# Optimization experiments

Measured on AMD Instinct MI355X. Metric: run time of the kernel, lower is better.

Reference implementation:

```python
import jax, jax.numpy as jnp
import numpy as np

B, C, H, W, NA = 2, 512, 25, 25, 9
A = H * W * NA  # 5625 anchors
PROB_T = 0.5
OVL_T = 0.5


def _make_anchors():
    ys, xs = np.meshgrid(np.arange(H), np.arange(W), indexing='ij')
    cx = (xs + 0.5) / W
    cy = (ys + 0.5) / H
    boxes = []
    for s in (0.1, 0.2, 0.4):
        for r in (0.5, 1.0, 2.0):
            w = s * np.sqrt(r)
            h = s / np.sqrt(r)
            boxes.append(np.stack([cx - w / 2, cy - h / 2, cx + w / 2, cy + h / 2], -1))
    anc = np.stack(boxes, axis=2)  # [H, W, 9, 4] matches [B,H,W,9*4] reshape order
    return jnp.asarray(anc.reshape(-1, 4), jnp.float32)


def setup_inputs() -> dict:
    key = jax.random.key(0)
    ks = jax.random.split(key, 4)
    x = jax.random.normal(ks[0], (B, C, H, W), jnp.float32)
    conv_w = jax.random.normal(ks[1], (512, 512, 3, 3), jnp.float32) * (1.0 / np.sqrt(512 * 9))
    conv_b = jnp.zeros((512,), jnp.float32)
    reg_w = jax.random.normal(ks[2], (36, 512), jnp.float32) * 0.02
    reg_b = jnp.zeros((36,), jnp.float32)
    cls_w = jax.random.normal(ks[3], (9, 512), jnp.float32) * 0.05
    cls_b = jnp.zeros((9,), jnp.float32)
    anchors = _make_anchors()
    return {"x": x, "conv_w": conv_w, "conv_b": conv_b, "reg_w": reg_w,
            "reg_b": reg_b, "cls_w": cls_w, "cls_b": cls_b, "anchors": anchors}


def reference(x, conv_w, conv_b, reg_w, reg_b, cls_w, cls_b, anchors):
    # --- RPN forward ---
    h = jax.lax.conv_general_dilated(x, conv_w, (1, 1), 'SAME',
                                     dimension_numbers=('NCHW', 'OIHW', 'NCHW'))
    h = jax.nn.relu(h + conv_b[None, :, None, None])
    box = jnp.einsum('bchw,oc->bhwo', h, reg_w) + reg_b  # [B,H,W,36] (== permute NHWC)
    cls = jnp.einsum('bchw,oc->bhwo', h, cls_w) + cls_b  # [B,H,W,9]
    offsets = box.reshape(B, A, 4)
    logits = cls.reshape(B, A)
    # --- detect: sigmoid + threshold ---
    probs = jax.nn.sigmoid(logits)
    valid = probs > PROB_T
    # --- box decode: gcxgcy -> cxcy -> xy (SSD-style, anchors given in xy) ---
    a_cx = (anchors[:, 0] + anchors[:, 2]) * 0.5
    a_cy = (anchors[:, 1] + anchors[:, 3]) * 0.5
    a_w = anchors[:, 2] - anchors[:, 0]
    a_h = anchors[:, 3] - anchors[:, 1]
    cx = offsets[..., 0] * a_w / 10.0 + a_cx
    cy = offsets[..., 1] * a_h / 10.0 + a_cy
    bw = jnp.exp(offsets[..., 2] / 5.0) * a_w
    bh = jnp.exp(offsets[..., 3] / 5.0) * a_h
    boxes = jnp.stack([cx - bw / 2, cy - bh / 2, cx + bw / 2, cy + bh / 2], -1)  # [B,A,4]
    # --- sort descending by score; invalid anchors sorted last and pre-suppressed ---
    sort_key = jnp.where(valid, probs, -1.0)
    order = jnp.argsort(-sort_key, axis=-1)
    sb = jnp.take_along_axis(boxes, order[..., None], axis=1)  # sorted boxes
    ss = jnp.take_along_axis(probs, order, axis=1)             # sorted scores
    sv = jnp.take_along_axis(valid, order, axis=1)             # sorted validity

    def per_image(b, v):
        x1, y1, x2, y2 = b[:, 0], b[:, 1], b[:, 2], b[:, 3]
        area = (x2 - x1) * (y2 - y1)
        iw = jnp.clip(jnp.minimum(x2[:, None], x2[None, :]) - jnp.maximum(x1[:, None], x1[None, :]), 0.0)
        ih = jnp.clip(jnp.minimum(y2[:, None], y2[None, :]) - jnp.maximum(y1[:, None], y1[None, :]), 0.0)
        inter = iw * ih
        ov = inter / (area[:, None] + area[None, :] - inter)  # [A,A] Jaccard
        sup0 = (~v).astype(jnp.int32)  # invalid anchors never considered

        def body(i, sup):
            cand = jnp.maximum(sup, (ov[i] > OVL_T).astype(jnp.int32)).at[i].set(0)
            return jnp.where(sup[i] > 0, sup, cand)  # skip if already suppressed

        sup = jax.lax.fori_loop(0, A, body, sup0)
        return (1 - sup) * v.astype(jnp.int32)

    keep = jax.vmap(per_image)(sb, sv)  # [B,A] 1 = kept detection
    return jnp.concatenate([sb, ss[..., None], keep[..., None].astype(jnp.float32)], -1)  # [B,A,6]
```

## Files before the change

kernel.cpp:

```cpp
#include <hip/hip_runtime.h>
#include <cstdint>
#include <cstddef>

#define AA 5625
#define MROWS 5760
#define ND 24

__global__ __launch_bounds__(256) void k_wt(const float* __restrict__ cw,
                                            float* __restrict__ wt,
                                            int* __restrict__ Vcnt) {
  if (blockIdx.x == 0 && threadIdx.x < 2) Vcnt[threadIdx.x] = 0;
  __shared__ float t[64][65];
  int kb = (blockIdx.x % 72) * 64;
  int ob = (blockIdx.x / 72) * 64;
  int col = threadIdx.x & 63;
  int rr  = threadIdx.x >> 6;
#pragma unroll
  for (int it = 0; it < 16; ++it) {
    int row = rr + it * 4;
    t[row][col] = cw[(size_t)(ob + row) * 4608 + kb + col];
  }
  __syncthreads();
#pragma unroll
  for (int it = 0; it < 16; ++it) {
    int row = rr + it * 4;
    wt[(size_t)(kb + row) * 512 + ob + col] = t[col][row];
  }
}

__global__ void k_xpad(const float* __restrict__ x, float* __restrict__ xp) {
  int n = blockIdx.x * 256 + threadIdx.x;
  if (n >= 884736) return;
  int c = n & 31;
  int r = (n >> 5) % 27;
  int rest = (n >> 5) / 27;
  float v = 0.f;
  int oy = r - 1, ox = c - 1;
  if (oy >= 0 && oy < 25 && ox >= 0 && ox < 25)
    v = x[(size_t)rest * 625 + oy * 25 + ox];
  xp[n] = v;
}

__global__ __launch_bounds__(256) void k_conv(const float* __restrict__ wt,
                                              const float* __restrict__ xp,
                                              double* __restrict__ hpart,
                                              int Kper) {
  int cpx = gridDim.x >> 3;
  int flat = blockIdx.x;
  int logical = (flat & 7) * cpx + (flat >> 3);
  int sharer = logical % 10;
  int s      = logical / 10;
  int Nt = s & 3;
  int ks = s >> 2;
  int b  = sharer / 5;
  int Mt = sharer % 5;

  int tid = threadIdx.x;
  int m0  = Mt * 128;
  int oc0 = Nt * 128;
  int R  = (tid >> 6) * 32 + ((tid >> 4) & 3) * 8;
  int cb = 2 * (tid & 15);

  __shared__ __align__(16) float As[2][18][128];
  __shared__ __align__(16) float Bs[2][18][128];

  double acc[8][8];
#pragma unroll
  for (int i = 0; i < 8; ++i)
#pragma unroll
    for (int j = 0; j < 8; ++j) acc[i][j] = 0.0;

  int kbase = ks * Kper;
  int nchunk = Kper / 18;

  int ldso[9];
  int boff[9];
  int aoff[9];
#pragma unroll
  for (int t = 0; t < 9; ++t) {
    int s2 = tid + 256 * t;
    int row = s2 >> 7, col = s2 & 127;
    ldso[t] = row * 128 + col;
    boff[t] = row * 512 + oc0 + col;
    int m = m0 + col;
    bool av = (m < 625);
    int mm = av ? m : 0;
    int icl = (row >= 9) ? 1 : 0;
    int tap = row - 9 * icl;
    int dy = tap / 3, dx = tap - 3 * dy;
    int yy = mm / 25, xx = mm - yy * 25;
    int ao = (icl * 27 + yy + dy) * 32 + xx + dx;
    aoff[t] = av ? ao : -1;
  }
  const float* wbase = wt + (size_t)kbase * 512;
  const float* abase = xp + (size_t)(b * 512 + kbase / 9) * 864;

  float rA[9], rB[9];

#define LOADCH(CH) {                                                          \
    int k0e = (CH) * (18 * 512);                                              \
    int a0e = (CH) * (2 * 864);                                               \
    _Pragma("unroll")                                                         \
    for (int t = 0; t < 9; ++t) {                                             \
      rB[t] = wbase[k0e + boff[t]];                                           \
      rA[t] = (aoff[t] >= 0) ? abase[a0e + aoff[t]] : 0.f;                    \
    } }
#define WRITECH(BUF) {                                                        \
    _Pragma("unroll")                                                         \
    for (int t = 0; t < 9; ++t) {                                             \
      ((float*)Bs[BUF])[ldso[t]] = rB[t];                                     \
      ((float*)As[BUF])[ldso[t]] = rA[t];                                     \
    } }

  LOADCH(0);
  WRITECH(0);
  __syncthreads();

  for (int ch = 0; ch < nchunk; ++ch) {
    int cur = ch & 1, nxt = cur ^ 1;
    int chn = (ch + 1 < nchunk) ? (ch + 1) : (nchunk - 1);
    LOADCH(chn);
#pragma unroll 2
    for (int kk = 0; kk < 18; ++kk) {
      float4 a0 = *(const float4*)&As[cur][kk][R];
      float4 a1 = *(const float4*)&As[cur][kk][R + 4];
      float2 b0 = *(const float2*)&Bs[cur][kk][cb];
      float2 b1 = *(const float2*)&Bs[cur][kk][cb + 32];
      float2 b2 = *(const float2*)&Bs[cur][kk][cb + 64];
      float2 b3 = *(const float2*)&Bs[cur][kk][cb + 96];
      double ad[8] = {(double)a0.x, (double)a0.y, (double)a0.z, (double)a0.w,
                      (double)a1.x, (double)a1.y, (double)a1.z, (double)a1.w};
      double bd[8] = {(double)b0.x, (double)b0.y, (double)b1.x, (double)b1.y,
                      (double)b2.x, (double)b2.y, (double)b3.x, (double)b3.y};
#pragma unroll
      for (int i = 0; i < 8; ++i)
#pragma unroll
        for (int j = 0; j < 8; ++j) acc[i][j] += ad[i] * bd[j];
    }
    if (ch + 1 < nchunk) {
      __syncthreads();
      WRITECH(nxt);
      __syncthreads();
    }
  }

  double* hb = hpart + ((size_t)(ks * 2 + b) * 625) * 512 + oc0 + cb;
#pragma unroll
  for (int i = 0; i < 8; ++i) {
    int mm = m0 + R + i;
    if (mm < 625) {
      double* p = hb + (size_t)mm * 512;
#pragma unroll
      for (int r = 0; r < 4; ++r) {
        double2 v; v.x = acc[i][2 * r]; v.y = acc[i][2 * r + 1];
        *(double2*)(p + 32 * r) = v;
      }
    }
  }
#undef LOADCH
#undef WRITECH
}

__device__ __forceinline__ double shfl_down_d(double x, int off) {
  long long v = __double_as_longlong(x);
  int lo = __shfl_down((int)(unsigned int)(v & 0xffffffffLL), off);
  int hi = __shfl_down((int)(v >> 32), off);
  return __longlong_as_double(((long long)hi << 32) | (unsigned int)lo);
}

__global__ __launch_bounds__(256) void k_heads(
    const double* __restrict__ hpart, const float* __restrict__ conv_b,
    const float* __restrict__ reg_w, const float* __restrict__ reg_b,
    const float* __restrict__ cls_w, const float* __restrict__ cls_b,
    const float* __restrict__ anchors, float* __restrict__ boxesraw,
    float* __restrict__ probs, unsigned long long* __restrict__ keys,
    unsigned int* __restrict__ rank, int nsplit) {
  int pos = blockIdx.x % 625;
  int b   = blockIdx.x / 625;
  int tid = threadIdx.x;
  __shared__ double hv[512];
  __shared__ double res[45];
  for (int c = tid; c < 512; c += 256) {
    double s = 0.0;
    for (int k = 0; k < nsplit; ++k)
      s += hpart[(((size_t)k * 2 + b) * 625 + pos) * 512 + c];
    s += (double)conv_b[c];
    hv[c] = s > 0.0 ? s : 0.0;
  }
  __syncthreads();
  int wv = tid >> 6, l = tid & 63;
  for (int o = wv; o < 45; o += 4) {
    const float* wrow = (o < 36) ? (reg_w + (size_t)o * 512)
                                 : (cls_w + (size_t)(o - 36) * 512);
    double s = 0.0;
#pragma unroll
    for (int kk = 0; kk < 8; ++kk)
      s += hv[l + kk * 64] * (double)wrow[l + kk * 64];
#pragma unroll
    for (int d = 32; d > 0; d >>= 1) s += shfl_down_d(s, d);
    if (l == 0) res[o] = s + (double)((o < 36) ? reg_b[o] : cls_b[o - 36]);
  }
  __syncthreads();
  if (tid < 9) {
    int na = tid;
    int a = pos * 9 + na;
    double o0 = res[na * 4 + 0], o1 = res[na * 4 + 1];
    double o2 = res[na * 4 + 2], o3 = res[na * 4 + 3];
    double logit = res[36 + na];
    float4 anc = *(const float4*)(anchors + (size_t)a * 4);
    double a_cx = ((double)anc.x + (double)anc.z) * 0.5;
    double a_cy = ((double)anc.y + (double)anc.w) * 0.5;
    double a_w = (double)anc.z - (double)anc.x;
    double a_h = (double)anc.w - (double)anc.y;
    double cx = o0 * a_w / 10.0 + a_cx;
    double cy = o1 * a_h / 10.0 + a_cy;
    double bw = exp(o2 / 5.0) * a_w;
    double bh = exp(o3 / 5.0) * a_h;
    float4 box = make_float4((float)(cx - bw / 2.0), (float)(cy - bh / 2.0),
                             (float)(cx + bw / 2.0), (float)(cy + bh / 2.0));
    size_t ga = (size_t)b * AA + a;
    *(float4*)(boxesraw + ga * 4) = box;
    float p = (float)(1.0 / (1.0 + exp(-logit)));
    probs[ga] = p;
    bool valid = p > 0.5f;
    float f = -(valid ? p : -1.0f);
    unsigned int u = __float_as_uint(f);
    u = (u & 0x80000000u) ? ~u : (u | 0x80000000u);
    keys[ga] = (((unsigned long long)u) << 32) | (unsigned int)a;
    rank[ga] = 0u;
  }
}

__global__ __launch_bounds__(256) void k_count(
    const unsigned long long* __restrict__ keys, unsigned int* __restrict__ rank) {
  int b = blockIdx.z;
  int i = blockIdx.x * 256 + threadIdx.x;
  __shared__ unsigned long long sj[1024];
  unsigned long long my = (i < AA) ? keys[(size_t)b * AA + i] : 0ULL;
  int j0 = blockIdx.y * 1024;
  for (int jj = threadIdx.x; jj < 1024; jj += 256) {
    int j = j0 + jj;
    sj[jj] = (j < AA) ? keys[(size_t)b * AA + j] : ~0ULL;
  }
  __syncthreads();
  int cnt = 0;
#pragma unroll 8
  for (int jj = 0; jj < 1024; ++jj) cnt += (sj[jj] < my) ? 1 : 0;
  if (i < AA && cnt) atomicAdd(&rank[(size_t)b * AA + i], (unsigned)cnt);
}

__global__ void k_perm(const unsigned long long* __restrict__ keys,
                       const unsigned int* __restrict__ rank,
                       unsigned int* __restrict__ perm, int* __restrict__ Vcnt) {
  int idx = blockIdx.x * 256 + threadIdx.x;
  if (idx >= 2 * AA) return;
  int b = idx / AA, i = idx - b * AA;
  unsigned long long k = keys[idx];
  unsigned int r = rank[idx];
  perm[(size_t)b * AA + r] = (unsigned)i;
  if (!(k >> 63)) atomicAdd(&Vcnt[b], 1);
}

__global__ void k_assembly(const unsigned int* __restrict__ perm,
                           const float* __restrict__ boxesraw,
                           const float* __restrict__ probs,
                           float* __restrict__ out, float4* __restrict__ sb4) {
  int idx = blockIdx.x * 256 + threadIdx.x;
  if (idx >= 2 * AA) return;
  int b = idx / AA;
  unsigned int pa = perm[idx];
  float4 bx = *(const float4*)(boxesraw + ((size_t)b * AA + pa) * 4);
  float p = probs[(size_t)b * AA + pa];
  float* o = out + (size_t)idx * 6;
  o[0] = bx.x; o[1] = bx.y; o[2] = bx.z; o[3] = bx.w; o[4] = p; o[5] = 0.f;
  sb4[idx] = bx;
}

__global__ __launch_bounds__(256) void k_maskT(const float4* __restrict__ sb4,
                                               const int* __restrict__ Vcnt,
                                               ulonglong2* __restrict__ maskT) {
  int b = blockIdx.y;
  int V = Vcnt[b];
  int i = blockIdx.x * 4 + (threadIdx.x >> 6);
  if (i >= V) return;
  int lane = threadIdx.x & 63;
  float4 bif = sb4[(size_t)b * AA + i];
  double bix = bif.x, biy = bif.y, biz = bif.z, biw = bif.w;
  double ai = (biz - bix) * (biw - biy);
  unsigned long long lo = 0, hi = 0;
#pragma unroll 4
  for (int w = 0; w < 88; ++w) {
    int j = w * 64 + lane;
    int jc = (j < AA) ? j : (AA - 1);
    float4 c = sb4[(size_t)b * AA + jc];
    double aj = ((double)c.z - (double)c.x) * ((double)c.w - (double)c.y);
    double iw = fmin(biz, (double)c.z) - fmax(bix, (double)c.x);
    double ih = fmin(biw, (double)c.w) - fmax(biy, (double)c.y);
    iw = iw > 0.0 ? iw : 0.0;
    ih = ih > 0.0 ? ih : 0.0;
    double inter = iw * ih;
    bool bit = (inter + inter > ai + aj - inter) && (j != i) && (j < AA);
    unsigned long long bb = bit ? 1ULL : 0ULL;
    if (w < 64) lo |= bb << w;
    else        hi |= bb << (w - 64);
  }
  ulonglong2 v; v.x = lo; v.y = hi;
  maskT[((size_t)b * MROWS + i) * 64 + lane] = v;
}

#define NMS_STEP(RING, I)                                                     \
  {                                                                           \
    int i = (I);                                                              \
    if (i < V) {                                                              \
      int w = i >> 6, t = i & 63;                                             \
      if (t == 0) {                                                           \
        unsigned long long cbit = (w < 64) ? (colLo >> w) : (colHi >> (w - 64)); \
        supw = __ballot((int)(cbit & 1ULL));                                  \
      }                                                                       \
      if (!((supw >> t) & 1ULL)) {                                            \
        colLo |= RING.x; colHi |= RING.y;                                     \
        unsigned long long cbit = (w < 64) ? (colLo >> w) : (colHi >> (w - 64)); \
        supw = __ballot((int)(cbit & 1ULL));                                  \
        if (lane == 0) out[((size_t)b * AA + i) * 6 + 5] = 1.0f;              \
      }                                                                       \
    }                                                                         \
  }

__global__ __launch_bounds__(64) void k_nms(const ulonglong2* __restrict__ maskT,
                                            const int* __restrict__ Vcnt,
                                            float* __restrict__ out) {
  int b = blockIdx.x;
  int lane = threadIdx.x;
  int V = Vcnt[b];
  const ulonglong2* mt = maskT + (size_t)b * MROWS * 64;
  unsigned long long colLo = 0, colHi = 0, supw = 0;
  ulonglong2 ra[ND], rb[ND];
#pragma unroll
  for (int j = 0; j < ND; ++j) ra[j] = mt[(size_t)j * 64 + lane];
#pragma unroll
  for (int j = 0; j < ND; ++j) rb[j] = mt[(size_t)(ND + j) * 64 + lane];
  for (int base = 0; base < V; base += 2 * ND) {
#pragma unroll
    for (int j = 0; j < ND; ++j) NMS_STEP(ra[j], base + j);
#pragma unroll
    for (int j = 0; j < ND; ++j) ra[j] = mt[(size_t)(base + 2 * ND + j) * 64 + lane];
#pragma unroll
    for (int j = 0; j < ND; ++j) NMS_STEP(rb[j], base + ND + j);
#pragma unroll
    for (int j = 0; j < ND; ++j) rb[j] = mt[(size_t)(base + 3 * ND + j) * 64 + lane];
  }
}
#undef NMS_STEP

extern "C" void kernel_launch(void* const* d_in, const int* in_sizes, int n_in,
                              void* d_out, int out_size, void* d_ws, size_t ws_size,
                              hipStream_t stream) {
  const float* x      = (const float*)d_in[0];
  const float* conv_w = (const float*)d_in[1];
  const float* conv_b = (const float*)d_in[2];
  const float* reg_w  = (const float*)d_in[3];
  const float* reg_b  = (const float*)d_in[4];
  const float* cls_w  = (const float*)d_in[5];
  const float* cls_b  = (const float*)d_in[6];
  const float* anchors= (const float*)d_in[7];
  float* out = (float*)d_out;
  char* ws = (char*)d_ws;

  size_t off = 0;
  auto alloc = [&](size_t bytes) {
    size_t o = off;
    off += (bytes + 255) & ~(size_t)255;
    return o;
  };
  size_t o_wt   = alloc(4608ULL * 512 * 4);
  size_t o_xp   = alloc(884736ULL * 4);
  size_t o_box  = alloc(2ULL * AA * 4 * 4);
  size_t o_prob = alloc(2ULL * AA * 4);
  size_t o_keys = alloc(2ULL * AA * 8);
  size_t o_rank = alloc(2ULL * AA * 4);
  size_t o_perm = alloc(2ULL * AA * 4);
  size_t o_sb4  = alloc(2ULL * AA * 16);
  size_t o_V    = alloc(256);
  size_t o_maskT= alloc(2ULL * MROWS * 64 * 16);
  size_t fixed = off;

  int nsplit = 1;
  const int cands[5] = {16, 8, 4, 2, 1};
  for (int ci = 0; ci < 5; ++ci) {
    size_t need = fixed + (size_t)cands[ci] * 2 * 625 * 512 * 8;
    if (need <= ws_size) { nsplit = cands[ci]; break; }
  }
  size_t o_hp = alloc((size_t)nsplit * 2 * 625 * 512 * 8);

  float* wtp   = (float*)(ws + o_wt);
  float* xpp   = (float*)(ws + o_xp);
  float* boxp  = (float*)(ws + o_box);
  float* probp = (float*)(ws + o_prob);
  unsigned long long* keysp = (unsigned long long*)(ws + o_keys);
  unsigned int* rankp = (unsigned int*)(ws + o_rank);
  unsigned int* permp = (unsigned int*)(ws + o_perm);
  float4* sb4p = (float4*)(ws + o_sb4);
  int* Vp      = (int*)(ws + o_V);
  ulonglong2* maskTp = (ulonglong2*)(ws + o_maskT);
  double* hpp  = (double*)(ws + o_hp);

  k_wt<<<dim3(576), dim3(256), 0, stream>>>(conv_w, wtp, Vp);
  k_xpad<<<dim3(3456), dim3(256), 0, stream>>>(x, xpp);
  k_conv<<<dim3(40 * nsplit), dim3(256), 0, stream>>>(wtp, xpp, hpp, 4608 / nsplit);
  k_heads<<<dim3(1250), dim3(256), 0, stream>>>(hpp, conv_b, reg_w, reg_b,
                                                cls_w, cls_b, anchors, boxp,
                                                probp, keysp, rankp, nsplit);
  k_count<<<dim3(22, 6, 2), dim3(256), 0, stream>>>(keysp, rankp);
  k_perm<<<dim3(44), dim3(256), 0, stream>>>(keysp, rankp, permp, Vp);
  k_assembly<<<dim3(44), dim3(256), 0, stream>>>(permp, boxp, probp, out, sb4p);
  k_maskT<<<dim3(1407, 2), dim3(256), 0, stream>>>(sb4p, Vp, maskTp);
  k_nms<<<dim3(2), dim3(64), 0, stream>>>(maskTp, Vp, out);
}
```

Before: 545.8 us.

## Merge prep kernels, split conv launch, unroll hpart reduction, rolling NMS prefetch

Fuses the weight transpose and input padding into one launch to drop a kernel launch. Splits the conv grid into two launches over halves of the K-splits, which adds a launch and may change CU scheduling. Unrolls the split-K partial sum in the heads kernel for the nsplit=16 case so the loads can be issued together. Replaces the NMS double-buffered register ring with a 32-deep rolling prefetch that reloads each slot right after use.

Result: slower. 586.8 us (+7.5%).

```diff
diff --git a/kernel.cpp b/kernel.cpp
--- a/kernel.cpp
+++ b/kernel.cpp
@@ -4,54 +4,55 @@
 
 #define AA 5625
 #define MROWS 5760
-#define ND 24
-
-__global__ __launch_bounds__(256) void k_wt(const float* __restrict__ cw,
-                                            float* __restrict__ wt,
-                                            int* __restrict__ Vcnt) {
-  if (blockIdx.x == 0 && threadIdx.x < 2) Vcnt[threadIdx.x] = 0;
-  __shared__ float t[64][65];
-  int kb = (blockIdx.x % 72) * 64;
-  int ob = (blockIdx.x / 72) * 64;
-  int col = threadIdx.x & 63;
-  int rr  = threadIdx.x >> 6;
-#pragma unroll
-  for (int it = 0; it < 16; ++it) {
-    int row = rr + it * 4;
-    t[row][col] = cw[(size_t)(ob + row) * 4608 + kb + col];
-  }
-  __syncthreads();
-#pragma unroll
-  for (int it = 0; it < 16; ++it) {
-    int row = rr + it * 4;
-    wt[(size_t)(kb + row) * 512 + ob + col] = t[col][row];
-  }
-}
-
-__global__ void k_xpad(const float* __restrict__ x, float* __restrict__ xp) {
-  int n = blockIdx.x * 256 + threadIdx.x;
-  if (n >= 884736) return;
-  int c = n & 31;
-  int r = (n >> 5) % 27;
-  int rest = (n >> 5) / 27;
-  float v = 0.f;
-  int oy = r - 1, ox = c - 1;
-  if (oy >= 0 && oy < 25 && ox >= 0 && ox < 25)
-    v = x[(size_t)rest * 625 + oy * 25 + ox];
-  xp[n] = v;
+
+__global__ __launch_bounds__(256) void k_prep(const float* __restrict__ cw,
+                                              const float* __restrict__ x,
+                                              float* __restrict__ wt,
+                                              float* __restrict__ xp,
+                                              int* __restrict__ Vcnt) {
+  if (blockIdx.x < 576) {
+    if (blockIdx.x == 0 && threadIdx.x < 2) Vcnt[threadIdx.x] = 0;
+    __shared__ float t[64][65];
+    int kb = (blockIdx.x % 72) * 64;
+    int ob = (blockIdx.x / 72) * 64;
+    int col = threadIdx.x & 63;
+    int rr  = threadIdx.x >> 6;
+#pragma unroll
+    for (int it = 0; it < 16; ++it) {
+      int row = rr + it * 4;
+      t[row][col] = cw[(size_t)(ob + row) * 4608 + kb + col];
+    }
+    __syncthreads();
+#pragma unroll
+    for (int it = 0; it < 16; ++it) {
+      int row = rr + it * 4;
+      wt[(size_t)(kb + row) * 512 + ob + col] = t[col][row];
+    }
+  } else {
+    int n = (blockIdx.x - 576) * 256 + threadIdx.x;
+    if (n >= 884736) return;
+    int c = n & 31;
+    int r = (n >> 5) % 27;
+    int rest = (n >> 5) / 27;
+    float v = 0.f;
+    int oy = r - 1, ox = c - 1;
+    if (oy >= 0 && oy < 25 && ox >= 0 && ox < 25)
+      v = x[(size_t)rest * 625 + oy * 25 + ox];
+    xp[n] = v;
+  }
 }
 
 __global__ __launch_bounds__(256) void k_conv(const float* __restrict__ wt,
                                               const float* __restrict__ xp,
                                               double* __restrict__ hpart,
-                                              int Kper) {
+                                              int Kper, int ksofs) {
   int cpx = gridDim.x >> 3;
   int flat = blockIdx.x;
   int logical = (flat & 7) * cpx + (flat >> 3);
   int sharer = logical % 10;
   int s      = logical / 10;
   int Nt = s & 3;
-  int ks = s >> 2;
+  int ks = (s >> 2) + ksofs;
   int b  = sharer / 5;
   int Mt = sharer % 5;
 
@@ -73,9 +74,7 @@
   int kbase = ks * Kper;
   int nchunk = Kper / 18;
 
-  int ldso[9];
-  int boff[9];
-  int aoff[9];
+  int ldso[9], aoff[9], boff[9];
 #pragma unroll
   for (int t = 0; t < 9; ++t) {
     int s2 = tid + 256 * t;
@@ -180,10 +179,24 @@
   int tid = threadIdx.x;
   __shared__ double hv[512];
   __shared__ double res[45];
+  const size_t kstr = (size_t)2 * 625 * 512;
   for (int c = tid; c < 512; c += 256) {
-    double s = 0.0;
-    for (int k = 0; k < nsplit; ++k)
-      s += hpart[(((size_t)k * 2 + b) * 625 + pos) * 512 + c];
+    const double* hp = hpart + ((size_t)b * 625 + pos) * 512 + c;
+    double s;
+    if (nsplit == 16) {
+      double t0 = hp[0],          t1 = hp[kstr],      t2 = hp[2 * kstr],
+             t3 = hp[3 * kstr],   t4 = hp[4 * kstr],  t5 = hp[5 * kstr],
+             t6 = hp[6 * kstr],   t7 = hp[7 * kstr],  t8 = hp[8 * kstr],
+             t9 = hp[9 * kstr],   t10 = hp[10 * kstr], t11 = hp[11 * kstr],
+             t12 = hp[12 * kstr], t13 = hp[13 * kstr], t14 = hp[14 * kstr],
+             t15 = hp[15 * kstr];
+      s = t0; s += t1; s += t2; s += t3; s += t4; s += t5; s += t6; s += t7;
+      s += t8; s += t9; s += t10; s += t11; s += t12; s += t13; s += t14;
+      s += t15;
+    } else {
+      s = 0.0;
+      for (int k = 0; k < nsplit; ++k) s += hp[(size_t)k * kstr];
+    }
     s += (double)conv_b[c];
     hv[c] = s > 0.0 ? s : 0.0;
   }
@@ -308,9 +321,9 @@
   maskT[((size_t)b * MROWS + i) * 64 + lane] = v;
 }
 
-#define NMS_STEP(RING, I)                                                     \
+#define NMS_STEP(Q, J)                                                        \
   {                                                                           \
-    int i = (I);                                                              \
+    int i = base + (J);                                                       \
     if (i < V) {                                                              \
       int w = i >> 6, t = i & 63;                                             \
       if (t == 0) {                                                           \
@@ -318,12 +331,13 @@
         supw = __ballot((int)(cbit & 1ULL));                                  \
       }                                                                       \
       if (!((supw >> t) & 1ULL)) {                                            \
-        colLo |= RING.x; colHi |= RING.y;                                     \
+        colLo |= Q.x; colHi |= Q.y;                                           \
         unsigned long long cbit = (w < 64) ? (colLo >> w) : (colHi >> (w - 64)); \
         supw = __ballot((int)(cbit & 1ULL));                                  \
         if (lane == 0) out[((size_t)b * AA + i) * 6 + 5] = 1.0f;              \
       }                                                                       \
     }                                                                         \
+    Q = mt[(size_t)(i + 32) * 64 + lane];                                     \
   }
 
 __global__ __launch_bounds__(64) void k_nms(const ulonglong2* __restrict__ maskT,
@@ -334,20 +348,31 @@
   int V = Vcnt[b];
   const ulonglong2* mt = maskT + (size_t)b * MROWS * 64;
   unsigned long long colLo = 0, colHi = 0, supw = 0;
-  ulonglong2 ra[ND], rb[ND];
-#pragma unroll
-  for (int j = 0; j < ND; ++j) ra[j] = mt[(size_t)j * 64 + lane];
-#pragma unroll
-  for (int j = 0; j < ND; ++j) rb[j] = mt[(size_t)(ND + j) * 64 + lane];
-  for (int base = 0; base < V; base += 2 * ND) {
-#pragma unroll
-    for (int j = 0; j < ND; ++j) NMS_STEP(ra[j], base + j);
-#pragma unroll
-    for (int j = 0; j < ND; ++j) ra[j] = mt[(size_t)(base + 2 * ND + j) * 64 + lane];
-#pragma unroll
-    for (int j = 0; j < ND; ++j) NMS_STEP(rb[j], base + ND + j);
-#pragma unroll
-    for (int j = 0; j < ND; ++j) rb[j] = mt[(size_t)(base + 3 * ND + j) * 64 + lane];
+  ulonglong2 q00 = mt[(size_t)0  * 64 + lane], q01 = mt[(size_t)1  * 64 + lane];
+  ulonglong2 q02 = mt[(size_t)2  * 64 + lane], q03 = mt[(size_t)3  * 64 + lane];
+  ulonglong2 q04 = mt[(size_t)4  * 64 + lane], q05 = mt[(size_t)5  * 64 + lane];
+  ulonglong2 q06 = mt[(size_t)6  * 64 + lane], q07 = mt[(size_t)7  * 64 + lane];
+  ulonglong2 q08 = mt[(size_t)8  * 64 + lane], q09 = mt[(size_t)9  * 64 + lane];
+  ulonglong2 q10 = mt[(size_t)10 * 64 + lane], q11 = mt[(size_t)11 * 64 + lane];
+  ulonglong2 q12 = mt[(size_t)12 * 64 + lane], q13 = mt[(size_t)13 * 64 + lane];
+  ulonglong2 q14 = mt[(size_t)14 * 64 + lane], q15 = mt[(size_t)15 * 64 + lane];
+  ulonglong2 q16 = mt[(size_t)16 * 64 + lane], q17 = mt[(size_t)17 * 64 + lane];
+  ulonglong2 q18 = mt[(size_t)18 * 64 + lane], q19 = mt[(size_t)19 * 64 + lane];
+  ulonglong2 q20 = mt[(size_t)20 * 64 + lane], q21 = mt[(size_t)21 * 64 + lane];
+  ulonglong2 q22 = mt[(size_t)22 * 64 + lane], q23 = mt[(size_t)23 * 64 + lane];
+  ulonglong2 q24 = mt[(size_t)24 * 64 + lane], q25 = mt[(size_t)25 * 64 + lane];
+  ulonglong2 q26 = mt[(size_t)26 * 64 + lane], q27 = mt[(size_t)27 * 64 + lane];
+  ulonglong2 q28 = mt[(size_t)28 * 64 + lane], q29 = mt[(size_t)29 * 64 + lane];
+  ulonglong2 q30 = mt[(size_t)30 * 64 + lane], q31 = mt[(size_t)31 * 64 + lane];
+  for (int base = 0; base < V; base += 32) {
+    NMS_STEP(q00, 0)  NMS_STEP(q01, 1)  NMS_STEP(q02, 2)  NMS_STEP(q03, 3)
+    NMS_STEP(q04, 4)  NMS_STEP(q05, 5)  NMS_STEP(q06, 6)  NMS_STEP(q07, 7)
+    NMS_STEP(q08, 8)  NMS_STEP(q09, 9)  NMS_STEP(q10, 10) NMS_STEP(q11, 11)
+    NMS_STEP(q12, 12) NMS_STEP(q13, 13) NMS_STEP(q14, 14) NMS_STEP(q15, 15)
+    NMS_STEP(q16, 16) NMS_STEP(q17, 17) NMS_STEP(q18, 18) NMS_STEP(q19, 19)
+    NMS_STEP(q20, 20) NMS_STEP(q21, 21) NMS_STEP(q22, 22) NMS_STEP(q23, 23)
+    NMS_STEP(q24, 24) NMS_STEP(q25, 25) NMS_STEP(q26, 26) NMS_STEP(q27, 27)
+    NMS_STEP(q28, 28) NMS_STEP(q29, 29) NMS_STEP(q30, 30) NMS_STEP(q31, 31)
   }
 }
 #undef NMS_STEP
@@ -404,9 +429,16 @@
   ulonglong2* maskTp = (ulonglong2*)(ws + o_maskT);
   double* hpp  = (double*)(ws + o_hp);
 
-  k_wt<<<dim3(576), dim3(256), 0, stream>>>(conv_w, wtp, Vp);
-  k_xpad<<<dim3(3456), dim3(256), 0, stream>>>(x, xpp);
-  k_conv<<<dim3(40 * nsplit), dim3(256), 0, stream>>>(wtp, xpp, hpp, 4608 / nsplit);
+  int Kper = 4608 / nsplit;
+
+  k_prep<<<dim3(4032), dim3(256), 0, stream>>>(conv_w, x, wtp, xpp, Vp);
+  if (nsplit > 1) {
+    int h = nsplit / 2;
+    k_conv<<<dim3(40 * h), dim3(256), 0, stream>>>(wtp, xpp, hpp, Kper, 0);
+    k_conv<<<dim3(40 * h), dim3(256), 0, stream>>>(wtp, xpp, hpp, Kper, h);
+  } else {
+    k_conv<<<dim3(40), dim3(256), 0, stream>>>(wtp, xpp, hpp, Kper, 0);
+  }
   k_heads<<<dim3(1250), dim3(256), 0, stream>>>(hpp, conv_b, reg_w, reg_b,
                                                 cls_w, cls_b, anchors, boxp,
                                                 probp, keysp, rankp, nsplit);
```
